# Optimization experiments

Hardware: AMD Instinct MI355X
Metric: run time of the kernel (lower is better)

Reference implementation:

```python
import jax, jax.numpy as jnp
import numpy as np

H_RENDER = 640   # hard-coded render resolution in the torch forward
W_RENDER = 640
OUT_H = 128      # self.height
OUT_W = 128      # self.width
NUM_VERTS = 778  # MANO hand mesh
NUM_FACES = 1538
BATCH = 4
BG_DEPTH = 1e10  # z-buffer background, clamped to 100 afterwards


def setup_inputs() -> dict:
    key = jax.random.key(0)
    k1, k2, k3 = jax.random.split(key, 3)
    # screen-space x,y in [0, 640), positive depth z
    xy = jax.random.uniform(k1, (BATCH, NUM_VERTS, 2), minval=0.0, maxval=640.0)
    z = jax.random.uniform(k2, (BATCH, NUM_VERTS, 1), minval=0.3, maxval=1.5)
    vertices = jnp.concatenate([xy, z], axis=-1).astype(jnp.float32)
    faces = jax.random.randint(k3, (NUM_FACES, 3), 0, NUM_VERTS)
    # right_hand=True: swap face columns 0 and 1 (winding flip), as in __init__
    faces = faces[:, jnp.array([1, 0, 2])].astype(jnp.int64)
    return {"vertices": vertices, "faces": faces}


def _edge(ax, ay, bx, by, px, py):
    # signed area of (a, b, p); standard rasterizer edge function
    return (bx - ax) * (py - ay) - (by - ay) * (px - ax)


def _rasterize(face_vertices):
    # face_vertices: [B, F, 3(vertex), 3(x,y,z)] -> z-buffer depth map [B, H, W]
    B = face_vertices.shape[0]
    ys, xs = jnp.meshgrid(
        jnp.arange(H_RENDER, dtype=jnp.float32) + 0.5,
        jnp.arange(W_RENDER, dtype=jnp.float32) + 0.5,
        indexing='ij',
    )  # pixel centers, [H, W]

    def step(zbuf, tri):
        # tri: [B, 3, 3] -> per-vertex coords broadcast to [B, 1, 1]
        x = tri[:, :, 0][:, :, None, None]
        y = tri[:, :, 1][:, :, None, None]
        z = tri[:, :, 2][:, :, None, None]
        x0, x1, x2 = x[:, 0], x[:, 1], x[:, 2]
        y0, y1, y2 = y[:, 0], y[:, 1], y[:, 2]
        z0, z1, z2 = z[:, 0], z[:, 1], z[:, 2]
        e0 = _edge(x1, y1, x2, y2, xs, ys)  # weight of v0
        e1 = _edge(x2, y2, x0, y0, xs, ys)  # weight of v1
        e2 = _edge(x0, y0, x1, y1, xs, ys)  # weight of v2
        area = _edge(x0, y0, x1, y1, x2, y2)  # [B,1,1]
        s = jnp.sign(area)
        valid = jnp.abs(area) > 1e-12
        inside = (e0 * s >= 0) & (e1 * s >= 0) & (e2 * s >= 0) & valid
        safe_area = jnp.where(valid, area, 1.0)
        zpix = (e0 * z0 + e1 * z1 + e2 * z2) / safe_area  # barycentric depth
        cand = jnp.where(inside, zpix, jnp.float32(BG_DEPTH))
        return jnp.minimum(zbuf, cand), None

    zbuf0 = jnp.full((B, H_RENDER, W_RENDER), BG_DEPTH, dtype=jnp.float32)
    zbuf, _ = jax.lax.scan(step, zbuf0, jnp.swapaxes(face_vertices, 0, 1))
    return zbuf


def reference(vertices, faces):
    B = vertices.shape[0]
    F = faces.shape[0]
    # vertex gather: vertices[:, faces.view(-1), 0:3].view(B, F, 3, 3)
    fv = vertices[:, faces.reshape(-1), 0:3].reshape(B, F, 3, 3)
    dm = _rasterize(fv)
    dm = jnp.minimum(dm, 100.0)  # torch.clamp(max=100.0)
    # bilinear resize, align_corners=False (half-pixel), no antialias, like F.interpolate
    resized = jax.image.resize(dm[:, None], (B, 1, OUT_H, OUT_W), method='linear', antialias=False)
    return resized[:, 0]
```

## Files before the change

### kernel.cpp

```cpp
#include <hip/hip_runtime.h>


#pragma clang fp contract(off)

#define H_OUT 128
#define W_OUT 128
#define NV 778
#define NF 1538
#define NB 4
#define NFP 1600
#define CAP 2048
#define BG100 0x42C80000u


__global__ __launch_bounds__(256) void prep_kernel(
    const float* __restrict__ verts,
    const int* __restrict__ faces,
    float* __restrict__ bbox,
    float* __restrict__ data,
    unsigned int* __restrict__ outu)
{
    int t = blockIdx.x * 256 + threadIdx.x;
    outu[t] = BG100;
    if (t >= NB * NFP) return;
    int b = t / NFP;
    int f = t - b * NFP;
    float* bb = bbox + (size_t)t * 4;
    float* o  = data + (size_t)t * 16;
    if (f >= NF) {
        bb[0] = 1e30f; bb[1] = -1e30f; bb[2] = 1e30f; bb[3] = -1e30f;
        o[0] = 0.0f; o[1] = 1.0f;
        o[2] = 0.0f; o[3] = 0.0f; o[4] = 0.0f; o[5] = 0.0f;
        o[6] = 0.0f; o[7] = 0.0f; o[8] = -1e30f; o[9] = 0.0f;
        o[10] = 0.0f; o[11] = 0.0f; o[12] = 0.0f; o[13] = 0.0f; o[14] = 0.0f;
        o[15] = 1.0f;
        return;
    }
    int i0 = faces[f * 3 + 0];
    int i1 = faces[f * 3 + 1];
    int i2 = faces[f * 3 + 2];
    const float* vb = verts + (size_t)b * NV * 3;
    float x0 = vb[i0 * 3 + 0], y0 = vb[i0 * 3 + 1], z0 = vb[i0 * 3 + 2];
    float x1 = vb[i1 * 3 + 0], y1 = vb[i1 * 3 + 1], z1 = vb[i1 * 3 + 2];
    float x2 = vb[i2 * 3 + 0], y2 = vb[i2 * 3 + 1], z2 = vb[i2 * 3 + 2];

    float dx12 = x2 - x1, dy12 = y2 - y1;
    float dx02 = x0 - x2, dy02 = y0 - y2;
    float dx01 = x1 - x0, dy01 = y1 - y0;
    float y20 = y2 - y0, x20 = x2 - x0;
    float area = dx01 * y20 - dy01 * x20;

    float s = 0.0f;
    if (fabsf(area) > 1e-12f) s = (area > 0.0f) ? 1.0f : -1.0f;

    float xmin = fminf(fminf(x0, x1), x2), xmax = fmaxf(fmaxf(x0, x1), x2);
    float ymin = fminf(fminf(y0, y1), y2), ymax = fmaxf(fmaxf(y0, y1), y2);
    if (s == 0.0f) { xmin = 1e30f; xmax = -1e30f; }

    bb[0] = xmin; bb[1] = xmax; bb[2] = ymin; bb[3] = ymax;

    o[0] = s * dx12; o[1] = s * dy12;
    o[2] = s * dx02; o[3] = s * dy02;
    o[4] = s * dx01; o[5] = s * dy01;
    o[6] = x0;  o[7] = y0;  o[8] = x1;  o[9] = y1;  o[10] = x2; o[11] = y2;
    o[12] = z0; o[13] = z1; o[14] = z2; o[15] = s * area;
}

__global__ __launch_bounds__(64) void bin_kernel(
    const float* __restrict__ bbox,
    unsigned int* __restrict__ list,
    unsigned int* __restrict__ count)
{
    int bin = blockIdx.x;
    int b = bin >> 6, tile = bin & 63;
    int tx = tile & 7, ty = tile >> 3;
    int lane = threadIdx.x;

    float px_lo = 80.0f * (float)tx + 2.5f, px_hi = px_lo + 75.0f;
    float py_lo = 80.0f * (float)ty + 2.5f, py_hi = py_lo + 75.0f;

    unsigned int* lp = list + (size_t)bin * CAP;
    unsigned int base = 0;
    for (int c = 0; c < NFP / 64; ++c) {
        int f = c * 64 + lane;
        float4 bb = *(const float4*)&bbox[(size_t)(b * NFP + f) * 4];
        bool ov = !(bb.x > px_hi || bb.y < px_lo ||
                    bb.z > py_hi || bb.w < py_lo);
        unsigned long long m = __ballot(ov);
        if (ov) {
            int pre = __popcll(m & ((1ull << lane) - 1ull));
            lp[base + pre] = (unsigned int)f;
        }
        base += (unsigned int)__popcll(m);
    }
    unsigned int padN = (32u - (base & 31u)) & 31u;
    if ((unsigned int)lane < padN) lp[base + lane] = NFP - 1;
    if (lane == 0) count[bin] = base + padN;
}

#define PIX(PY, NBv, ABv)                                                   \
    {                                                                       \
        float e0 = A.x * ((PY) - C.y) - hx0;                                \
        float e1 = A.z * ((PY) - C.w) - hx1;                                \
        float e2 = B.x * ((PY) - B.w) - hx2;                                \
        bool ins = (e0 >= 0.0f) & (e1 >= 0.0f) & (e2 >= 0.0f);              \
        float n = ((e0 * D.x) + (e1 * D.y)) + (e2 * D.z);                   \
        bool tk = ins & (n * (ABv) < (NBv) * D.w);                          \
        NBv = tk ? n : (NBv);  ABv = tk ? D.w : (ABv);                      \
    }

#define FACE(IDX)                                                           \
    {                                                                       \
        const float4* _p =                                                  \
            (const float4*)(data + (size_t)(gb + (int)(IDX)) * 16);         \
        float4 A = _p[0], B = _p[1], C = _p[2], D = _p[3];                  \
        float hx0 = A.y * (px - C.x);                                       \
        float hx1 = A.w * (px - C.z);                                       \
        float hx2 = B.y * (px - B.z);                                       \
        PIX(py0, nb0, ab0)                                                  \
        PIX(py1, nb1, ab1)                                                  \
        PIX(py2, nb2, ab2)                                                  \
        PIX(py3, nb3, ab3)                                                  \
    }

__global__ __launch_bounds__(128) void raster_kernel(
    const float* __restrict__ data,
    const unsigned int* __restrict__ list,
    const unsigned int* __restrict__ count,
    unsigned int* __restrict__ outu)
{
    int blk = blockIdx.x;
    int bin = blk & 255;
    int pp  = blk >> 8;
    int tid = threadIdx.x;
    int w = __builtin_amdgcn_readfirstlane(tid >> 6);
    int piece = pp * 2 + w;

    unsigned int cnt = count[bin];
    if ((unsigned int)(piece * 32) >= cnt) return;

    int b = bin >> 6, tile = bin & 63;
    int tx = tile & 7, ty = tile >> 3;
    int lane = tid & 63;
    int col = lane & 15;
    int rg  = lane >> 4;
    int j = tx * 16 + col;
    int i0r = ty * 16 + rg;
    float px  = 5.0f * (float)j + 2.5f;
    float py0 = 5.0f * (float)i0r + 2.5f;
    float py1 = py0 + 20.0f, py2 = py0 + 40.0f, py3 = py0 + 60.0f;
    int gb = b * NFP;

    const unsigned int* lp = list + (size_t)bin * CAP + piece * 32;

    float nb0 = 1e10f, ab0 = 1.0f;
    float nb1 = 1e10f, ab1 = 1.0f;
    float nb2 = 1e10f, ab2 = 1.0f;
    float nb3 = 1e10f, ab3 = 1.0f;

    for (int q = 0; q < 8; ++q) {
        uint4 I = *(const uint4*)(lp + q * 4);
        FACE(I.x)
        FACE(I.y)
        FACE(I.z)
        FACE(I.w)
    }

    unsigned int* slot0 = &outu[(size_t)b * (H_OUT * W_OUT) + i0r * W_OUT + j];
    {
        float z = nb0 / ab0; z += 0.0f;
        if (z < 1e9f) atomicMin(slot0, __float_as_uint(fminf(z, 100.0f)));
    }
    {
        float z = nb1 / ab1; z += 0.0f;
        if (z < 1e9f) atomicMin(slot0 + 4 * W_OUT, __float_as_uint(fminf(z, 100.0f)));
    }
    {
        float z = nb2 / ab2; z += 0.0f;
        if (z < 1e9f) atomicMin(slot0 + 8 * W_OUT, __float_as_uint(fminf(z, 100.0f)));
    }
    {
        float z = nb3 / ab3; z += 0.0f;
        if (z < 1e9f) atomicMin(slot0 + 12 * W_OUT, __float_as_uint(fminf(z, 100.0f)));
    }
}

extern "C" void kernel_launch(void* const* d_in, const int* in_sizes, int n_in,
                              void* d_out, int out_size, void* d_ws, size_t ws_size,
                              hipStream_t stream) {
    const float* verts = (const float*)d_in[0];
    const int*   faces = (const int*)d_in[1];
    float* out = (float*)d_out;
    float* bbox = (float*)d_ws;
    float* data = bbox + (size_t)NB * NFP * 4;
    unsigned int* list = (unsigned int*)(data + (size_t)NB * NFP * 16);
    unsigned int* count = list + (size_t)256 * CAP;

    prep_kernel<<<256, 256, 0, stream>>>(verts, faces, bbox, data,
                                         (unsigned int*)out);
    bin_kernel<<<256, 64, 0, stream>>>(bbox, list, count);
    raster_kernel<<<32 * 256, 128, 0, stream>>>(
        data, list, count, (unsigned int*)out);
}
```

Measured before the change: 101.9 us.

## Pack binned face data per tile and stage it through LDS in raster

The binning kernel now copies each overlapping face's full 64-byte record into a per-bin packed buffer instead of writing face indices. The raster kernel loads its 32-face chunk with two coalesced float4 loads per lane into shared memory and reads the records from LDS. This removes the dependent index-then-gather global loads in the inner loop. In exchange the bin kernel writes about 16x more data, the workspace grows by 32 MB, and there is no barrier between the LDS write and the reads, relying on the data being per-wavefront.

```diff
diff --git a/kernel.cpp b/kernel.cpp
--- a/kernel.cpp
+++ b/kernel.cpp
@@ -68,33 +68,43 @@
 
 __global__ __launch_bounds__(64) void bin_kernel(
     const float* __restrict__ bbox,
-    unsigned int* __restrict__ list,
+    const float* __restrict__ data,
+    float* __restrict__ packed,
     unsigned int* __restrict__ count)
 {
     int bin = blockIdx.x;
     int b = bin >> 6, tile = bin & 63;
     int tx = tile & 7, ty = tile >> 3;
     int lane = threadIdx.x;
+    int gb = b * NFP;
 
     float px_lo = 80.0f * (float)tx + 2.5f, px_hi = px_lo + 75.0f;
     float py_lo = 80.0f * (float)ty + 2.5f, py_hi = py_lo + 75.0f;
 
-    unsigned int* lp = list + (size_t)bin * CAP;
+    float* pk = packed + (size_t)bin * CAP * 16;
     unsigned int base = 0;
     for (int c = 0; c < NFP / 64; ++c) {
         int f = c * 64 + lane;
-        float4 bb = *(const float4*)&bbox[(size_t)(b * NFP + f) * 4];
+        float4 bb = *(const float4*)&bbox[(size_t)(gb + f) * 4];
         bool ov = !(bb.x > px_hi || bb.y < px_lo ||
                     bb.z > py_hi || bb.w < py_lo);
         unsigned long long m = __ballot(ov);
         if (ov) {
             int pre = __popcll(m & ((1ull << lane) - 1ull));
-            lp[base + pre] = (unsigned int)f;
+            const float4* src = (const float4*)(data + (size_t)(gb + f) * 16);
+            float4 r0 = src[0], r1 = src[1], r2 = src[2], r3 = src[3];
+            float4* dst = (float4*)(pk + (size_t)(base + pre) * 16);
+            dst[0] = r0; dst[1] = r1; dst[2] = r2; dst[3] = r3;
         }
         base += (unsigned int)__popcll(m);
     }
     unsigned int padN = (32u - (base & 31u)) & 31u;
-    if ((unsigned int)lane < padN) lp[base + lane] = NFP - 1;
+    if ((unsigned int)lane < padN) {
+        const float4* src = (const float4*)(data + (size_t)(gb + NFP - 1) * 16);
+        float4 r0 = src[0], r1 = src[1], r2 = src[2], r3 = src[3];
+        float4* dst = (float4*)(pk + (size_t)(base + lane) * 16);
+        dst[0] = r0; dst[1] = r1; dst[2] = r2; dst[3] = r3;
+    }
     if (lane == 0) count[bin] = base + padN;
 }
 
@@ -109,26 +119,13 @@
         NBv = tk ? n : (NBv);  ABv = tk ? D.w : (ABv);                      \
     }
 
-#define FACE(IDX)                                                           \
-    {                                                                       \
-        const float4* _p =                                                  \
-            (const float4*)(data + (size_t)(gb + (int)(IDX)) * 16);         \
-        float4 A = _p[0], B = _p[1], C = _p[2], D = _p[3];                  \
-        float hx0 = A.y * (px - C.x);                                       \
-        float hx1 = A.w * (px - C.z);                                       \
-        float hx2 = B.y * (px - B.z);                                       \
-        PIX(py0, nb0, ab0)                                                  \
-        PIX(py1, nb1, ab1)                                                  \
-        PIX(py2, nb2, ab2)                                                  \
-        PIX(py3, nb3, ab3)                                                  \
-    }
-
 __global__ __launch_bounds__(128) void raster_kernel(
-    const float* __restrict__ data,
-    const unsigned int* __restrict__ list,
+    const float* __restrict__ packed,
     const unsigned int* __restrict__ count,
     unsigned int* __restrict__ outu)
 {
+    __shared__ float lds[2][32 * 16];
+
     int blk = blockIdx.x;
     int bin = blk & 255;
     int pp  = blk >> 8;
@@ -139,9 +136,16 @@
     unsigned int cnt = count[bin];
     if ((unsigned int)(piece * 32) >= cnt) return;
 
+    int lane = tid & 63;
+    const float4* src =
+        (const float4*)(packed + ((size_t)bin * CAP + (size_t)piece * 32) * 16);
+    float4 s0 = src[lane], s1 = src[lane + 64];
+    float* L = lds[w];
+    ((float4*)L)[lane]      = s0;
+    ((float4*)L)[lane + 64] = s1;
+
     int b = bin >> 6, tile = bin & 63;
     int tx = tile & 7, ty = tile >> 3;
-    int lane = tid & 63;
     int col = lane & 15;
     int rg  = lane >> 4;
     int j = tx * 16 + col;
@@ -149,21 +153,23 @@
     float px  = 5.0f * (float)j + 2.5f;
     float py0 = 5.0f * (float)i0r + 2.5f;
     float py1 = py0 + 20.0f, py2 = py0 + 40.0f, py3 = py0 + 60.0f;
-    int gb = b * NFP;
-
-    const unsigned int* lp = list + (size_t)bin * CAP + piece * 32;
 
     float nb0 = 1e10f, ab0 = 1.0f;
     float nb1 = 1e10f, ab1 = 1.0f;
     float nb2 = 1e10f, ab2 = 1.0f;
     float nb3 = 1e10f, ab3 = 1.0f;
 
-    for (int q = 0; q < 8; ++q) {
-        uint4 I = *(const uint4*)(lp + q * 4);
-        FACE(I.x)
-        FACE(I.y)
-        FACE(I.z)
-        FACE(I.w)
+    #pragma unroll 4
+    for (int f = 0; f < 32; ++f) {
+        const float4* p = (const float4*)&L[f * 16];
+        float4 A = p[0], B = p[1], C = p[2], D = p[3];
+        float hx0 = A.y * (px - C.x);
+        float hx1 = A.w * (px - C.z);
+        float hx2 = B.y * (px - B.z);
+        PIX(py0, nb0, ab0)
+        PIX(py1, nb1, ab1)
+        PIX(py2, nb2, ab2)
+        PIX(py3, nb3, ab3)
     }
 
     unsigned int* slot0 = &outu[(size_t)b * (H_OUT * W_OUT) + i0r * W_OUT + j];
@@ -193,12 +199,13 @@
     float* out = (float*)d_out;
     float* bbox = (float*)d_ws;
     float* data = bbox + (size_t)NB * NFP * 4;
-    unsigned int* list = (unsigned int*)(data + (size_t)NB * NFP * 16);
-    unsigned int* count = list + (size_t)256 * CAP;
+    float* packed = data + (size_t)NB * NFP * 16;
+    unsigned int* count =
+        (unsigned int*)(packed + (size_t)256 * CAP * 16);
 
     prep_kernel<<<256, 256, 0, stream>>>(verts, faces, bbox, data,
                                          (unsigned int*)out);
-    bin_kernel<<<256, 64, 0, stream>>>(bbox, list, count);
+    bin_kernel<<<256, 64, 0, stream>>>(bbox, data, packed, count);
     raster_kernel<<<32 * 256, 128, 0, stream>>>(
-        data, list, count, (unsigned int*)out);
-}
+        packed, count, (unsigned int*)out);
+}
```

Result: slower. 118.0 us (+15.8%).
